# Kernel tuning notes

Hardware: AMD Instinct MI355X
Metric: run time of the kernel (lower is better)

The kernel has to match this reference:

```python
import jax, jax.numpy as jnp
import numpy as np

B, S, E = 4, 1024, 1024   # batch, seq_len, emb_dim
H = 8                      # num_head
D = E                      # in_emb_dim defaults to emb_dim
NEG = -9e15                # source uses -9000000000000000.0


def setup_inputs() -> dict:
    key = jax.random.key(0)
    kq, kk, kv, kwq, kwk, kwv, kwl = jax.random.split(key, 7)
    q = jax.random.normal(kq, (B, S, E), dtype=jnp.float32)
    k = jax.random.normal(kk, (B, S, E), dtype=jnp.float32)
    v = jax.random.normal(kv, (B, S, E), dtype=jnp.float32)
    # Per-head Linear(emb_dim -> in_emb_dim, bias=False) weights, torch layout [out, in]
    Wq = jax.random.normal(kwq, (H, D, E), dtype=jnp.float32) * 0.02
    Wk = jax.random.normal(kwk, (H, D, E), dtype=jnp.float32) * 0.02
    Wv = jax.random.normal(kwv, (H, D, E), dtype=jnp.float32) * 0.02
    # last_dense: Linear(in_emb_dim*num_head -> emb_dim, bias=False)
    Wlast = jax.random.normal(kwl, (E, H * D), dtype=jnp.float32) * 0.02
    return {"q": q, "k": k, "v": v, "Wq": Wq, "Wk": Wk, "Wv": Wv, "Wlast": Wlast}


def reference(q, k, v, Wq, Wk, Wv, Wlast):
    # batched per-head projections: y = x @ W[h].T  -> [B,H,S,D]
    in_q = jnp.einsum('bse,hde->bhsd', q, Wq)
    in_k = jnp.einsum('bse,hde->bhsd', k, Wk)
    in_v = jnp.einsum('bse,hde->bhsd', v, Wv)
    # faithful: scaled by sqrt(kv sequence length), not head dim
    scale = 1.0 / jnp.sqrt(jnp.float32(k.shape[-2]))
    logits = jnp.einsum('bhqd,bhkd->bhqk', in_q, in_k) * scale
    # source maps exactly-zero logits to -9e15 before softmax
    logits = jnp.where(logits != 0, logits, jnp.full_like(logits, NEG))
    atten = jax.nn.softmax(logits, axis=-1)          # [B,H,Sq,Sk]
    out_h = jnp.einsum('bhqk,bhkd->bhqd', atten, in_v)
    # concat heads along last dim in head order (matches torch.cat loop)
    b, h, sq, d = out_h.shape
    h_cat = out_h.transpose(0, 2, 1, 3).reshape(b, sq, h * d)
    return jnp.einsum('bsf,ef->bse', h_cat, Wlast)   # last_dense, bias=False
```

## Files before the change

kernel.cpp:

```cpp
#include <hip/hip_runtime.h>
#include <stdint.h>

typedef _Float16 f16;
typedef _Float16 f16x8 __attribute__((ext_vector_type(8)));
typedef _Float16 f16x4 __attribute__((ext_vector_type(4)));
typedef float f32x4 __attribute__((ext_vector_type(4)));

__device__ __forceinline__ void gload_lds16(const void* g, void* l) {
    __builtin_amdgcn_global_load_lds(
        (const __attribute__((address_space(1))) unsigned int*)g,
        (__attribute__((address_space(3))) unsigned int*)l, 16, 0, 0);
}

#define VMWAIT0() asm volatile("s_waitcnt vmcnt(0)" ::: "memory")
#define LGKM0()   asm volatile("s_waitcnt lgkmcnt(0)" ::: "memory")

struct Cvt4 {
    const float* s[4];
    f16* d[4];
    int n8[4];
};
__global__ __launch_bounds__(256) void cvt_plain4(Cvt4 c) {
    const int seg = blockIdx.y;
    const int i = blockIdx.x * 256 + threadIdx.x;
    if (i >= c.n8[seg]) return;
    const float4* s4 = (const float4*)c.s[seg];
    float4 a = s4[2 * (size_t)i];
    float4 b = s4[2 * (size_t)i + 1];
    f16x8 o;
    o[0] = (f16)a.x; o[1] = (f16)a.y; o[2] = (f16)a.z; o[3] = (f16)a.w;
    o[4] = (f16)b.x; o[5] = (f16)b.y; o[6] = (f16)b.z; o[7] = (f16)b.w;
    *(f16x8*)(c.d[seg] + (size_t)i * 8) = o;
}

struct T3 { const float* s[3]; f16* d[3]; };
__global__ __launch_bounds__(256) void cvt_transpose3(T3 c) {
    const int bid = blockIdx.x;
    const int dt = bid & 15;
    const int et = (bid >> 4) & 15;
    const int zz = bid >> 8;
    const int m = zz >> 3, h = zz & 7;
    const float* src = c.s[m] + (size_t)h * 1048576;
    f16* dst = c.d[m] + (size_t)h * 1048576;
    __shared__ f16 t[64][72];
    const int r  = threadIdx.x >> 2;
    const int cq = threadIdx.x & 3;
    const int d0 = dt * 64, e0 = et * 64;
#pragma unroll
    for (int i = 0; i < 4; ++i) {
        const int cc = cq * 4 + i * 16;
        float4 vv = *(const float4*)(src + (size_t)(d0 + r) * 1024 + e0 + cc);
        t[cc + 0][r] = (f16)vv.x;
        t[cc + 1][r] = (f16)vv.y;
        t[cc + 2][r] = (f16)vv.z;
        t[cc + 3][r] = (f16)vv.w;
    }
    __syncthreads();
#pragma unroll
    for (int i = 0; i < 4; ++i) {
        const int cc = cq * 4 + i * 16;
        f16x4 w;
        w[0] = t[r][cc + 0];
        w[1] = t[r][cc + 1];
        w[2] = t[r][cc + 2];
        w[3] = t[r][cc + 3];
        *(f16x4*)(dst + (size_t)(e0 + r) * 1024 + d0 + cc) = w;
    }
}

template <typename OutT>
__global__ __launch_bounds__(256, 2) void gemm_bt(
    const f16* __restrict__ A, const f16* __restrict__ B, OutT* __restrict__ C,
    int ldA, int ldB, long long ldC, int K, float alpha,
    long long sAh, long long sAb, long long sBh, long long sBb,
    long long sCh, long long sCb, int NB) {
    const int z = blockIdx.z;
    const int h = z / NB, bb = z % NB;
    A += h * sAh + bb * sAb;
    B += h * sBh + bb * sBb;
    C += h * sCh + bb * sCb;

    const int row0 = blockIdx.y * 128;
    const int col0 = blockIdx.x * 128;

    __shared__ __align__(16) f16 smA[128 * 64];
    __shared__ __align__(16) f16 smB[128 * 64];

    const int tid  = threadIdx.x;
    const int lane = tid & 63;
    const int wid  = tid >> 6;
    const int wr   = (wid >> 1) * 64;
    const int wc   = (wid & 1) * 64;
    const int fr   = lane & 15;
    const int fkb  = (lane >> 4) * 16;

    f32x4 acc[4][4] = {};

    const int nkt = K >> 6;
    for (int kt = 0; kt < nkt; ++kt) {
#pragma unroll
        for (int it = 0; it < 4; ++it) {
            int p = (it * 256 + tid) * 16;
            int n = p ^ (((p >> 7) & 7) << 4);
            int r   = n >> 7;
            int kel = (n & 127) >> 1;
            size_t ga = (size_t)(row0 + r) * (size_t)ldA + (size_t)(kt * 64 + kel);
            gload_lds16(A + ga, (char*)smA + p);
            size_t gb = (size_t)(col0 + r) * (size_t)ldB + (size_t)(kt * 64 + kel);
            gload_lds16(B + gb, (char*)smB + p);
        }
        __syncthreads();

#pragma unroll
        for (int ks = 0; ks < 2; ++ks) {
            f16x8 af[4], bf[4];
#pragma unroll
            for (int i = 0; i < 4; ++i) {
                int rowA = wr + i * 16 + fr;
                int na   = rowA * 128 + ks * 64 + fkb;
                af[i] = *(const f16x8*)((const char*)smA + (na ^ ((rowA & 7) << 4)));
                int rowB = wc + i * 16 + fr;
                int nb   = rowB * 128 + ks * 64 + fkb;
                bf[i] = *(const f16x8*)((const char*)smB + (nb ^ ((rowB & 7) << 4)));
            }
#pragma unroll
            for (int i = 0; i < 4; ++i)
#pragma unroll
                for (int j = 0; j < 4; ++j)
                    acc[i][j] = __builtin_amdgcn_mfma_f32_16x16x32_f16(
                        af[i], bf[j], acc[i][j], 0, 0, 0);
        }
        __syncthreads();
    }

    const int er = (lane >> 4) * 4;
#pragma unroll
    for (int i = 0; i < 4; ++i)
#pragma unroll
        for (int j = 0; j < 4; ++j)
#pragma unroll
            for (int r = 0; r < 4; ++r) {
                size_t idx = (size_t)(row0 + wr + i * 16 + er + r) * (size_t)ldC +
                             (size_t)(col0 + wc + j * 16 + fr);
                C[idx] = (OutT)(acc[i][j][r] * alpha);
            }
}

template <typename OutT>
__global__ __launch_bounds__(512, 2) void gemm2ph(
    const f16* __restrict__ A, const f16* __restrict__ B, OutT* __restrict__ C,
    int ldA, int ldB, long long ldC, int K, float alpha,
    long long sAh, long long sAb, long long sBh, long long sBb,
    long long sCh, long long sCb, int NB, int gx, int gy) {
    extern __shared__ char lds[];

    const int nwg = gridDim.x;
    const int q = nwg >> 3, r = nwg & 7;
    const int xcd = blockIdx.x & 7, lid = blockIdx.x >> 3;
    const int wg = (xcd < r ? xcd * (q + 1) : r * (q + 1) + (xcd - r) * q) + lid;
    const int z = wg / (gx * gy);
    const int rem = wg - z * (gx * gy);
    const int by = rem / gx, bx = rem - by * gx;
    const int h = z / NB, bb = z - h * NB;
    A += h * sAh + bb * sAb;
    B += h * sBh + bb * sBb;
    C += h * sCh + bb * sCb;
    const int row0 = by * 256, col0 = bx * 256;

    const int tid  = threadIdx.x;
    const int lane = tid & 63;
    const int wid  = tid >> 6;
    const int wm   = wid >> 2;
    const int wn   = wid & 3;
    const int fr   = lane & 15;
    const int fkb  = (lane >> 4) << 4;
    const int sw0  = fkb ^ ((fr & 7) << 4);
    const int sw1  = sw0 ^ 64;

    const unsigned ldsbase = (unsigned)(uintptr_t)(char*)lds;
    const unsigned aRow = ldsbase + (unsigned)((wm * 128 + fr) * 128);
    const unsigned bRow = ldsbase + 32768u + (unsigned)((wn * 64 + fr) * 128);

    const int srow  = tid >> 3;
    const int scol  = (((tid & 7) ^ ((tid >> 3) & 7)) << 4) >> 1;
    const f16* gA = A + (size_t)(row0 + srow) * ldA + scol;
    const f16* gB = B + (size_t)(col0 + srow) * ldB + scol;
    char* lA = (char*)lds + tid * 16;
    char* lB = lA + 32768;

    const int nkt = K >> 6;

#define STAGE(tt, bufo) do { \
        const size_t _ko = (size_t)(tt) * 64; \
        gload_lds16(gA + _ko,                        lA + (bufo)); \
        gload_lds16(gA + 64  * (size_t)ldA + _ko,    lA + (bufo) + 8192); \
        gload_lds16(gA + 128 * (size_t)ldA + _ko,    lA + (bufo) + 16384); \
        gload_lds16(gA + 192 * (size_t)ldA + _ko,    lA + (bufo) + 24576); \
        gload_lds16(gB + _ko,                        lB + (bufo)); \
        gload_lds16(gB + 64  * (size_t)ldB + _ko,    lB + (bufo) + 8192); \
        gload_lds16(gB + 128 * (size_t)ldB + _ko,    lB + (bufo) + 16384); \
        gload_lds16(gB + 192 * (size_t)ldB + _ko,    lB + (bufo) + 24576); \
    } while (0)

#define DSR2(r0, r1, addr, o0, o1) \
    asm volatile("ds_read_b128 %0, %2 offset:" #o0 "\n\t" \
                 "ds_read_b128 %1, %2 offset:" #o1 \
                 : "=&v"(r0), "=&v"(r1) : "v"(addr))

#define MF(i, j, av, bv) \
    acc[i][j] = __builtin_amdgcn_mfma_f32_16x16x32_f16(av, bv, acc[i][j], 0, 0, 0)

#define HALF(sw) do { \
        f16x8 a0, a1, a2, a3, a4, a5, a6, a7, b0, b1, b2, b3; \
        const unsigned aA = aRow + bo + (sw); \
        const unsigned aB = bRow + bo + (sw); \
        DSR2(a0, a1, aA, 0, 2048); \
        DSR2(a2, a3, aA, 4096, 6144); \
        DSR2(a4, a5, aA, 8192, 10240); \
        DSR2(a6, a7, aA, 12288, 14336); \
        DSR2(b0, b1, aB, 0, 2048); \
        DSR2(b2, b3, aB, 4096, 6144); \
        LGKM0(); \
        __builtin_amdgcn_sched_barrier(0); \
        __builtin_amdgcn_s_setprio(1); \
        MF(0,0,a0,b0); MF(0,1,a0,b1); MF(0,2,a0,b2); MF(0,3,a0,b3); \
        MF(1,0,a1,b0); MF(1,1,a1,b1); MF(1,2,a1,b2); MF(1,3,a1,b3); \
        MF(2,0,a2,b0); MF(2,1,a2,b1); MF(2,2,a2,b2); MF(2,3,a2,b3); \
        MF(3,0,a3,b0); MF(3,1,a3,b1); MF(3,2,a3,b2); MF(3,3,a3,b3); \
        MF(4,0,a4,b0); MF(4,1,a4,b1); MF(4,2,a4,b2); MF(4,3,a4,b3); \
        MF(5,0,a5,b0); MF(5,1,a5,b1); MF(5,2,a5,b2); MF(5,3,a5,b3); \
        MF(6,0,a6,b0); MF(6,1,a6,b1); MF(6,2,a6,b2); MF(6,3,a6,b3); \
        MF(7,0,a7,b0); MF(7,1,a7,b1); MF(7,2,a7,b2); MF(7,3,a7,b3); \
        __builtin_amdgcn_s_setprio(0); \
    } while (0)

    STAGE(0, 0);
    VMWAIT0();
    __builtin_amdgcn_s_barrier();

    f32x4 acc[8][4] = {};
    unsigned cur = 0;

    for (int t = 0; t < nkt; ++t) {
        const unsigned bo = cur << 16;
        if (t + 1 < nkt) STAGE(t + 1, bo ^ 65536u);
        HALF(sw0);
        HALF(sw1);
        VMWAIT0();
        __builtin_amdgcn_s_barrier();
        cur ^= 1;
    }
#undef HALF
#undef MF
#undef DSR2
#undef STAGE

    const int er = (lane >> 4) * 4;
#pragma unroll
    for (int i = 0; i < 8; ++i)
#pragma unroll
        for (int j = 0; j < 4; ++j)
#pragma unroll
            for (int rr = 0; rr < 4; ++rr) {
                size_t idx = (size_t)(row0 + wm * 128 + i * 16 + er + rr) * (size_t)ldC +
                             (size_t)(col0 + wn * 64 + j * 16 + fr);
                C[idx] = (OutT)(acc[i][j][rr] * alpha);
            }
}

__global__ __launch_bounds__(256) void reduce_split2(const float* __restrict__ p,
                                                     float* __restrict__ o, int n4) {
    int i = blockIdx.x * 256 + threadIdx.x;
    if (i >= n4) return;
    const int b  = i >> 18;
    const int jj = i & 262143;
    const float4* p4 = (const float4*)p;
    const size_t base = (size_t)b * 524288 + jj;
    float4 a = p4[base], c = p4[base + 262144];
    float4 s;
    s.x = a.x + c.x;
    s.y = a.y + c.y;
    s.z = a.z + c.z;
    s.w = a.w + c.w;
    ((float4*)o)[i] = s;
}

__global__ __launch_bounds__(256) void softmax_rows(f16* __restrict__ P) {
    const size_t row = blockIdx.x;
    f16* p = P + row * 1024;
    const int tid = threadIdx.x, lane = tid & 63, wid = tid >> 6;

    f16x4 v4 = *(const f16x4*)(p + tid * 4);
    float v[4];
#pragma unroll
    for (int t = 0; t < 4; ++t) {
        v[t] = (float)v4[t];
        if (v[t] == 0.0f) v[t] = -9e15f;
    }
    float m = fmaxf(fmaxf(v[0], v[1]), fmaxf(v[2], v[3]));
#pragma unroll
    for (int o = 32; o > 0; o >>= 1) m = fmaxf(m, __shfl_xor(m, o));
    __shared__ float red[8];
    if (lane == 0) red[wid] = m;
    __syncthreads();
    m = fmaxf(fmaxf(red[0], red[1]), fmaxf(red[2], red[3]));

    float e[4], s = 0.f;
#pragma unroll
    for (int t = 0; t < 4; ++t) { e[t] = __expf(v[t] - m); s += e[t]; }
#pragma unroll
    for (int o = 32; o > 0; o >>= 1) s += __shfl_xor(s, o);
    if (lane == 0) red[4 + wid] = s;
    __syncthreads();
    s = red[4] + red[5] + red[6] + red[7];
    float inv = 1.0f / s;

    f16x4 o4;
#pragma unroll
    for (int t = 0; t < 4; ++t) o4[t] = (f16)(e[t] * inv);
    *(f16x4*)(p + tid * 4) = o4;
}

extern "C" void kernel_launch(void* const* d_in, const int* in_sizes, int n_in,
                              void* d_out, int out_size, void* d_ws, size_t ws_size,
                              hipStream_t stream) {
    const float* q  = (const float*)d_in[0];
    const float* k  = (const float*)d_in[1];
    const float* v  = (const float*)d_in[2];
    const float* Wq = (const float*)d_in[3];
    const float* Wk = (const float*)d_in[4];
    const float* Wv = (const float*)d_in[5];
    const float* Wl = (const float*)d_in[6];
    float* out = (float*)d_out;

    (void)hipFuncSetAttribute((const void*)gemm2ph<f16>,
                              hipFuncAttributeMaxDynamicSharedMemorySize, 131072);

    const size_t MB = 1024ull * 1024ull;
    char* ws = (char*)d_ws;
    f16*  q_h  = (f16*)(ws + 0 * MB);
    f16*  k_h  = (f16*)(ws + 8 * MB);
    f16*  v_h  = (f16*)(ws + 16 * MB);
    f16*  Wl_h = (f16*)(ws + 24 * MB);
    f16*  WqT  = (f16*)(ws + 40 * MB);
    f16*  WkT  = (f16*)(ws + 56 * MB);
    f16*  WvT  = (f16*)(ws + 72 * MB);
    f16*  Mt   = (f16*)(ws + 88 * MB);
    f16*  G    = (f16*)(ws + 104 * MB);
    f16*  Aq   = (f16*)(ws + 24 * MB);
    f16*  P    = (f16*)(ws + 120 * MB);
    f16*  Xt   = (f16*)(ws + 24 * MB);
    float* part = (float*)(ws + 88 * MB);

    Cvt4 c4;
    c4.s[0] = q;  c4.d[0] = q_h;  c4.n8[0] = 524288;
    c4.s[1] = k;  c4.d[1] = k_h;  c4.n8[1] = 524288;
    c4.s[2] = v;  c4.d[2] = v_h;  c4.n8[2] = 524288;
    c4.s[3] = Wl; c4.d[3] = Wl_h; c4.n8[3] = 1048576;
    cvt_plain4<<<dim3(4096, 4), 256, 0, stream>>>(c4);

    T3 t3;
    t3.s[0] = Wq; t3.d[0] = WqT;
    t3.s[1] = Wk; t3.d[1] = WkT;
    t3.s[2] = Wv; t3.d[2] = WvT;
    cvt_transpose3<<<6144, 256, 0, stream>>>(t3);

    const long long M1 = 1048576ll;
    const long long M8 = 8388608ll;
    const float SCALE = 0.03125f;
    dim3 blk(256);
    const size_t SMEM = 131072;

    gemm_bt<f16><<<dim3(8, 8, 8), blk, 0, stream>>>(
        WkT, WqT, Mt, 1024, 1024, 1024, 1024, 1.0f,
        M1, 0, M1, 0, M1, 0, 1);
    gemm_bt<f16><<<dim3(8, 8, 8), blk, 0, stream>>>(
        Wl_h, WvT, G, 8192, 1024, 1024, 1024, 1.0f,
        1024, 0, M1, 0, M1, 0, 1);
    gemm2ph<f16><<<512, 512, SMEM, stream>>>(
        q_h, Mt, Aq, 1024, 1024, 1024, 1024, 1.0f,
        0, M1, M1, 0, 4 * M1, M1, 4, 4, 4);
    gemm2ph<f16><<<512, 512, SMEM, stream>>>(
        Aq, k_h, P, 1024, 1024, 8192, 1024, SCALE,
        4 * M1, M1, 0, M1, 1024, M8, 4, 4, 4);
    gemm2ph<f16><<<512, 512, SMEM, stream>>>(
        G, v_h, Xt, 1024, 1024, 8192, 1024, 1.0f,
        M1, 0, 0, M1, 1024, M8, 4, 4, 4);
    softmax_rows<<<32768, 256, 0, stream>>>(P);
    gemm_bt<float><<<dim3(8, 8, 8), blk, 0, stream>>>(
        P, Xt, part, 8192, 8192, 1024, 4096, 1.0f,
        M8, 4096, M8, 4096, 2 * M1, M1, 2);
    reduce_split2<<<4096, 256, 0, stream>>>(part, out, 1048576);
}
```

Measured before the change: 435.3 us.

## Restructure 256x256 GEMM into eight-phase pipelined loop with split-K LDS staging

Replaces the two-phase double-buffered GEMM main loop with an eight-phase schedule. Each 64-wide K tile is split into two 32-wide halves, and the A and B loads are issued in quarter-sized chunks interleaved with MFMA groups. Partial vmcnt waits (vmcnt(8)) let global-to-LDS loads stay in flight across phases, and the LDS layout and swizzle change to 64-byte rows for the half-K tiles. The aim is to overlap memory traffic with MFMA work and avoid full-drain waits, at the cost of many more workgroup barriers per iteration and more fragile vmcnt accounting.

Result: slower. 450.5 us (+3.5%).

```diff
diff --git a/kernel.cpp b/kernel.cpp
--- a/kernel.cpp
+++ b/kernel.cpp
@@ -12,6 +12,7 @@
         (__attribute__((address_space(3))) unsigned int*)l, 16, 0, 0);
 }
 
+#define VMWAIT8() asm volatile("s_waitcnt vmcnt(8)" ::: "memory")
 #define VMWAIT0() asm volatile("s_waitcnt vmcnt(0)" ::: "memory")
 #define LGKM0()   asm volatile("s_waitcnt lgkmcnt(0)" ::: "memory")
 
@@ -147,7 +148,7 @@
 }
 
 template <typename OutT>
-__global__ __launch_bounds__(512, 2) void gemm2ph(
+__global__ __launch_bounds__(512, 2) void gemm8p(
     const f16* __restrict__ A, const f16* __restrict__ B, OutT* __restrict__ C,
     int ldA, int ldB, long long ldC, int K, float alpha,
     long long sAh, long long sAb, long long sBh, long long sBb,
@@ -173,16 +174,14 @@
     const int wm   = wid >> 2;
     const int wn   = wid & 3;
     const int fr   = lane & 15;
-    const int fkb  = (lane >> 4) << 4;
-    const int sw0  = fkb ^ ((fr & 7) << 4);
-    const int sw1  = sw0 ^ 64;
+    const int swz  = ((lane >> 4) << 4) ^ (((fr >> 1) & 3) << 4);
 
     const unsigned ldsbase = (unsigned)(uintptr_t)(char*)lds;
-    const unsigned aRow = ldsbase + (unsigned)((wm * 128 + fr) * 128);
-    const unsigned bRow = ldsbase + 32768u + (unsigned)((wn * 64 + fr) * 128);
-
-    const int srow  = tid >> 3;
-    const int scol  = (((tid & 7) ^ ((tid >> 3) & 7)) << 4) >> 1;
+    const unsigned aBase = ldsbase + (unsigned)((wm * 128 + fr) * 64 + swz);
+    const unsigned bBase = ldsbase + 32768u + (unsigned)((wn * 64 + fr) * 64 + swz);
+
+    const int srow = tid >> 2;
+    const int scol = (((tid & 3) << 4) ^ (((srow >> 1) & 3) << 4)) >> 1;
     const f16* gA = A + (size_t)(row0 + srow) * ldA + scol;
     const f16* gB = B + (size_t)(col0 + srow) * ldB + scol;
     char* lA = (char*)lds + tid * 16;
@@ -190,16 +189,15 @@
 
     const int nkt = K >> 6;
 
-#define STAGE(tt, bufo) do { \
-        const size_t _ko = (size_t)(tt) * 64; \
-        gload_lds16(gA + _ko,                        lA + (bufo)); \
-        gload_lds16(gA + 64  * (size_t)ldA + _ko,    lA + (bufo) + 8192); \
-        gload_lds16(gA + 128 * (size_t)ldA + _ko,    lA + (bufo) + 16384); \
-        gload_lds16(gA + 192 * (size_t)ldA + _ko,    lA + (bufo) + 24576); \
-        gload_lds16(gB + _ko,                        lB + (bufo)); \
-        gload_lds16(gB + 64  * (size_t)ldB + _ko,    lB + (bufo) + 8192); \
-        gload_lds16(gB + 128 * (size_t)ldB + _ko,    lB + (bufo) + 16384); \
-        gload_lds16(gB + 192 * (size_t)ldB + _ko,    lB + (bufo) + 24576); \
+#define STG_A(tt, kh, bo) do { \
+        const size_t _ko = (size_t)(tt) * 64 + (kh) * 32; \
+        gload_lds16(gA + _ko,                     lA + (bo) + (kh) * 16384); \
+        gload_lds16(gA + 128 * (size_t)ldA + _ko, lA + (bo) + (kh) * 16384 + 8192); \
+    } while (0)
+#define STG_B(tt, kh, bo) do { \
+        const size_t _ko = (size_t)(tt) * 64 + (kh) * 32; \
+        gload_lds16(gB + _ko,                     lB + (bo) + (kh) * 16384); \
+        gload_lds16(gB + 128 * (size_t)ldB + _ko, lB + (bo) + (kh) * 16384 + 8192); \
     } while (0)
 
 #define DSR2(r0, r1, addr, o0, o1) \
@@ -210,50 +208,77 @@
 #define MF(i, j, av, bv) \
     acc[i][j] = __builtin_amdgcn_mfma_f32_16x16x32_f16(av, bv, acc[i][j], 0, 0, 0)
 
-#define HALF(sw) do { \
-        f16x8 a0, a1, a2, a3, a4, a5, a6, a7, b0, b1, b2, b3; \
-        const unsigned aA = aRow + bo + (sw); \
-        const unsigned aB = bRow + bo + (sw); \
-        DSR2(a0, a1, aA, 0, 2048); \
-        DSR2(a2, a3, aA, 4096, 6144); \
-        DSR2(a4, a5, aA, 8192, 10240); \
-        DSR2(a6, a7, aA, 12288, 14336); \
-        DSR2(b0, b1, aB, 0, 2048); \
-        DSR2(b2, b3, aB, 4096, 6144); \
-        LGKM0(); \
-        __builtin_amdgcn_sched_barrier(0); \
+#define MFMA16(i0) do { \
         __builtin_amdgcn_s_setprio(1); \
-        MF(0,0,a0,b0); MF(0,1,a0,b1); MF(0,2,a0,b2); MF(0,3,a0,b3); \
-        MF(1,0,a1,b0); MF(1,1,a1,b1); MF(1,2,a1,b2); MF(1,3,a1,b3); \
-        MF(2,0,a2,b0); MF(2,1,a2,b1); MF(2,2,a2,b2); MF(2,3,a2,b3); \
-        MF(3,0,a3,b0); MF(3,1,a3,b1); MF(3,2,a3,b2); MF(3,3,a3,b3); \
-        MF(4,0,a4,b0); MF(4,1,a4,b1); MF(4,2,a4,b2); MF(4,3,a4,b3); \
-        MF(5,0,a5,b0); MF(5,1,a5,b1); MF(5,2,a5,b2); MF(5,3,a5,b3); \
-        MF(6,0,a6,b0); MF(6,1,a6,b1); MF(6,2,a6,b2); MF(6,3,a6,b3); \
-        MF(7,0,a7,b0); MF(7,1,a7,b1); MF(7,2,a7,b2); MF(7,3,a7,b3); \
+        MF(i0+0,0,a0,b0); MF(i0+0,1,a0,b1); MF(i0+0,2,a0,b2); MF(i0+0,3,a0,b3); \
+        MF(i0+1,0,a1,b0); MF(i0+1,1,a1,b1); MF(i0+1,2,a1,b2); MF(i0+1,3,a1,b3); \
+        MF(i0+2,0,a2,b0); MF(i0+2,1,a2,b1); MF(i0+2,2,a2,b2); MF(i0+2,3,a2,b3); \
+        MF(i0+3,0,a3,b0); MF(i0+3,1,a3,b1); MF(i0+3,2,a3,b2); MF(i0+3,3,a3,b3); \
         __builtin_amdgcn_s_setprio(0); \
     } while (0)
 
-    STAGE(0, 0);
-    VMWAIT0();
+    STG_A(0, 0, 0); STG_B(0, 0, 0);
+    STG_A(0, 1, 0); STG_B(0, 1, 0);
+    if (nkt > 1) { STG_A(1, 0, 65536); STG_B(1, 0, 65536); }
+    VMWAIT8();
     __builtin_amdgcn_s_barrier();
 
     f32x4 acc[8][4] = {};
-    unsigned cur = 0;
+    f16x8 a0, a1, a2, a3, b0, b1, b2, b3;
 
     for (int t = 0; t < nkt; ++t) {
-        const unsigned bo = cur << 16;
-        if (t + 1 < nkt) STAGE(t + 1, bo ^ 65536u);
-        HALF(sw0);
-        HALF(sw1);
-        VMWAIT0();
-        __builtin_amdgcn_s_barrier();
-        cur ^= 1;
+        const unsigned bo  = (unsigned)((t & 1) << 16);
+        const unsigned bo2 = bo ^ 65536u;
+        const unsigned aA = aBase + bo, aB = bBase + bo;
+
+        if (t + 1 < nkt) STG_A(t + 1, 1, bo2);
+        DSR2(a0, a1, aA, 0, 1024);
+        DSR2(a2, a3, aA, 2048, 3072);
+        DSR2(b0, b1, aB, 0, 1024);
+        DSR2(b2, b3, aB, 2048, 3072);
+        __builtin_amdgcn_s_barrier();
+        LGKM0();
+        __builtin_amdgcn_sched_barrier(0);
+        MFMA16(0);
+        __builtin_amdgcn_s_barrier();
+
+        if (t + 1 < nkt) STG_B(t + 1, 1, bo2);
+        DSR2(a0, a1, aA, 4096, 5120);
+        DSR2(a2, a3, aA, 6144, 7168);
+        __builtin_amdgcn_s_barrier();
+        LGKM0();
+        __builtin_amdgcn_sched_barrier(0);
+        MFMA16(4);
+        __builtin_amdgcn_s_barrier();
+        VMWAIT8();
+
+        if (t + 2 < nkt) STG_A(t + 2, 0, bo);
+        DSR2(a0, a1, aA, 16384, 17408);
+        DSR2(a2, a3, aA, 18432, 19456);
+        DSR2(b0, b1, aB, 16384, 17408);
+        DSR2(b2, b3, aB, 18432, 19456);
+        __builtin_amdgcn_s_barrier();
+        LGKM0();
+        __builtin_amdgcn_sched_barrier(0);
+        MFMA16(0);
+        __builtin_amdgcn_s_barrier();
+
+        if (t + 2 < nkt) STG_B(t + 2, 0, bo);
+        DSR2(a0, a1, aA, 20480, 21504);
+        DSR2(a2, a3, aA, 22528, 23552);
+        __builtin_amdgcn_s_barrier();
+        LGKM0();
+        __builtin_amdgcn_sched_barrier(0);
+        MFMA16(4);
+        if (t == nkt - 2) VMWAIT0();
+        else              VMWAIT8();
+        __builtin_amdgcn_s_barrier();
     }
-#undef HALF
+#undef MFMA16
 #undef MF
 #undef DSR2
-#undef STAGE
+#undef STG_A
+#undef STG_B
 
     const int er = (lane >> 4) * 4;
 #pragma unroll
@@ -333,7 +358,7 @@
     const float* Wl = (const float*)d_in[6];
     float* out = (float*)d_out;
 
-    (void)hipFuncSetAttribute((const void*)gemm2ph<f16>,
+    (void)hipFuncSetAttribute((const void*)gemm8p<f16>,
                               hipFuncAttributeMaxDynamicSharedMemorySize, 131072);
 
     const size_t MB = 1024ull * 1024ull;
@@ -377,13 +402,13 @@
     gemm_bt<f16><<<dim3(8, 8, 8), blk, 0, stream>>>(
         Wl_h, WvT, G, 8192, 1024, 1024, 1024, 1.0f,
         1024, 0, M1, 0, M1, 0, 1);
-    gemm2ph<f16><<<512, 512, SMEM, stream>>>(
+    gemm8p<f16><<<512, 512, SMEM, stream>>>(
         q_h, Mt, Aq, 1024, 1024, 1024, 1024, 1.0f,
         0, M1, M1, 0, 4 * M1, M1, 4, 4, 4);
-    gemm2ph<f16><<<512, 512, SMEM, stream>>>(
+    gemm8p<f16><<<512, 512, SMEM, stream>>>(
         Aq, k_h, P, 1024, 1024, 8192, 1024, SCALE,
         4 * M1, M1, 0, M1, 1024, M8, 4, 4, 4);
-    gemm2ph<f16><<<512, 512, SMEM, stream>>>(
+    gemm8p<f16><<<512, 512, SMEM, stream>>>(
         G, v_h, Xt, 1024, 1024, 8192, 1024, 1.0f,
         M1, 0, 0, M1, 1024, M8, 4, 4, 4);
     softmax_rows<<<32768, 256, 0, stream>>>(P);
```
